# Performance work log

Hardware: AMD Instinct MI355X
Metric: run time of the kernel (lower is better)

Reference implementation:

```python
import jax, jax.numpy as jnp
import numpy as np

D_MODEL = 1024
T = 4096

def setup_inputs() -> dict:
    key = jax.random.key(0)
    k1, k2, k3 = jax.random.split(key, 3)
    x = jax.random.normal(k1, (T, D_MODEL), dtype=jnp.float32)
    # original uses torch.rand (uniform [0,1)) for params
    Wqk = jax.random.uniform(k2, (D_MODEL, D_MODEL), dtype=jnp.float32)
    Wov = jax.random.uniform(k3, (D_MODEL, D_MODEL), dtype=jnp.float32)
    return {"x": x, "Wqk": Wqk, "Wov": Wov}

def reference(x, Wqk, Wov):
    Tcur = x.shape[0]
    # scores = softmax(x @ Wqk @ x^T + causal_mask)
    q = x @ Wqk                              # [T, d]
    logits = q @ x.T                         # [T, T]
    causal = jnp.tril(jnp.ones((Tcur, Tcur), dtype=bool))
    logits = jnp.where(causal, logits, -jnp.inf)
    attn = jax.nn.softmax(logits, axis=-1)   # [T, T]
    out = (attn @ x) @ Wov                   # [T, d]
    return out
```

## Files before the change

kernel.cpp:

```cpp
#include <hip/hip_runtime.h>
#include <hip/hip_fp16.h>

#define T_DIM 4096
#define D_DIM 1024

typedef _Float16 f16;
typedef _Float16 f16x4 __attribute__((ext_vector_type(4)));
typedef _Float16 f16x8 __attribute__((ext_vector_type(8)));
typedef float f32x4 __attribute__((ext_vector_type(4)));

#define GAS __attribute__((address_space(1)))
#define LAS __attribute__((address_space(3)))

__global__ void split4(const float* __restrict__ in, f16* __restrict__ hi,
                       f16* __restrict__ lo) {
    int i = (blockIdx.x * 256 + threadIdx.x) * 4;
    float4 v = *(const float4*)(in + i);
    float vv[4] = {v.x, v.y, v.z, v.w};
    f16x4 h, l;
#pragma unroll
    for (int j = 0; j < 4; ++j) {
        f16 hh = (f16)vv[j];
        h[j] = hh;
        l[j] = (f16)(vv[j] - (float)hh);
    }
    *(f16x4*)(hi + i) = h;
    *(f16x4*)(lo + i) = l;
}

__global__ void transpose_split(const float* __restrict__ in, f16* __restrict__ hi,
                                f16* __restrict__ lo, int R, int C) {
    __shared__ float t[32][33];
    int tx = threadIdx.x & 31;
    int ty = threadIdx.x >> 5;
#pragma unroll
    for (int q = 0; q < 4; ++q) {
        int r = blockIdx.y * 32 + ty + q * 8;
        int c = blockIdx.x * 32 + tx;
        t[ty + q * 8][tx] = in[(size_t)r * C + c];
    }
    __syncthreads();
#pragma unroll
    for (int q = 0; q < 4; ++q) {
        int c = blockIdx.x * 32 + ty + q * 8;
        int r = blockIdx.y * 32 + tx;
        float v = t[tx][ty + q * 8];
        size_t idx = (size_t)c * R + r;
        f16 h = (f16)v;
        hi[idx] = h;
        lo[idx] = (f16)(v - (float)h);
    }
}

template <int ROWS>
__device__ __forceinline__ void stage_tile(const f16* __restrict__ src, int ld,
                                           f16* lds_tile, int w, int l) {
    constexpr int ITER = (ROWS * 4) / 256;
#pragma unroll
    for (int q = 0; q < ITER; ++q) {
        int p = q * 256 + w * 64 + l;
        int r = p >> 2;
        int c = (p & 3) ^ ((r >> 1) & 3);
        const f16* g = src + r * ld + c * 8;
        f16* d = lds_tile + (q * 256 + w * 64) * 8;
        __builtin_amdgcn_global_load_lds((const GAS void*)g, (LAS void*)d, 16, 0, 0);
    }
}

template <int N>
__device__ __forceinline__ void vm_wait() {
    static_assert(N == 0 || N == 3 || N == 6 || N == 8, "unsupported vmcnt");
    if constexpr (N == 0) asm volatile("s_waitcnt vmcnt(0)" ::: "memory");
    else if constexpr (N == 3) asm volatile("s_waitcnt vmcnt(3)" ::: "memory");
    else if constexpr (N == 6) asm volatile("s_waitcnt vmcnt(6)" ::: "memory");
    else if constexpr (N == 8) asm volatile("s_waitcnt vmcnt(8)" ::: "memory");
}

template <int TM, int TN, bool SPLIT3, int OUT_MODE, bool CAUSAL_SKIP,
          bool KCAP_CAUSAL, bool REVY>
__global__ __launch_bounds__(256) void gemm_nt(
    const f16* __restrict__ Ah, const f16* __restrict__ Al,
    const f16* __restrict__ Bh, const f16* __restrict__ Bl,
    float* __restrict__ Cf, f16* __restrict__ Ch, f16* __restrict__ Cl,
    int M, int N, int K) {
    const int by = REVY ? (gridDim.y - 1 - blockIdx.y) : blockIdx.y;
    const int row0 = by * TM;
    const int col0 = blockIdx.x * TN;
    if (CAUSAL_SKIP) {
        if (col0 > row0 + TM - 1) return;
    }
    int Keff = K;
    if (KCAP_CAUSAL) {
        Keff = row0 + TM;
        if (Keff > K) Keff = K;
    }

    constexpr int TILE_A = TM * 32;
    constexpr int TILE_B = TN * 32;
    constexpr int BUFSZ = (SPLIT3 ? 2 : 1) * (TILE_A + TILE_B);
    constexpr int M_REP = TM / 32;
    constexpr int N_REP = TN / 32;
    constexpr int LPS = (SPLIT3 ? 2 : 1) * (TM + TN) / 64;
    __shared__ f16 lds[2 * BUFSZ];

    const int tid = threadIdx.x;
    const int w = tid >> 6, l = tid & 63;
    const int wm = w >> 1, wn = w & 1;
    const int lr = l & 15;
    const int kg = l >> 4;
    const int cswz = kg ^ ((lr >> 1) & 3);
    const int aoff = (wm * (TM / 2) + lr) * 32 + cswz * 8;
    const int boff = (wn * (TN / 2) + lr) * 32 + cswz * 8;

    const f16* Asrc = Ah + (size_t)row0 * K;
    const f16* Bsrc = Bh + (size_t)col0 * K;
    const f16* Asrc_l = SPLIT3 ? Al + (size_t)row0 * K : nullptr;
    const f16* Bsrc_l = SPLIT3 ? Bl + (size_t)col0 * K : nullptr;

    auto stage_all = [&](int buf, int k0) {
        f16* base = lds + buf * BUFSZ;
        stage_tile<TM>(Asrc + k0, K, base, w, l);
        stage_tile<TN>(Bsrc + k0, K, base + TILE_A, w, l);
        if constexpr (SPLIT3) {
            stage_tile<TM>(Asrc_l + k0, K, base + TILE_A + TILE_B, w, l);
            stage_tile<TN>(Bsrc_l + k0, K, base + 2 * TILE_A + TILE_B, w, l);
        }
    };

    f32x4 acc[M_REP][N_REP] = {};

    const int nsteps = Keff >> 5;

    stage_all(0, 0);
    stage_all(1, 32);

    int cur = 0;
    for (int i = 0; i < nsteps; ++i) {
        if (i + 1 < nsteps) vm_wait<LPS>(); else vm_wait<0>();
        __builtin_amdgcn_sched_barrier(0);
        __builtin_amdgcn_s_barrier();
        __builtin_amdgcn_sched_barrier(0);

        const f16* base = lds + cur * BUFSZ;
        const f16* Ah_t = base;
        const f16* Bh_t = base + TILE_A;
        const f16* Al_t = base + TILE_A + TILE_B;
        const f16* Bl_t = base + 2 * TILE_A + TILE_B;

        f16x8 ah[M_REP], bh[N_REP], al[M_REP], bl[N_REP];
#pragma unroll
        for (int m = 0; m < M_REP; ++m) {
            ah[m] = *(const f16x8*)&Ah_t[aoff + m * 512];
            if constexpr (SPLIT3) al[m] = *(const f16x8*)&Al_t[aoff + m * 512];
        }
#pragma unroll
        for (int n = 0; n < N_REP; ++n) {
            bh[n] = *(const f16x8*)&Bh_t[boff + n * 512];
            if constexpr (SPLIT3) bl[n] = *(const f16x8*)&Bl_t[boff + n * 512];
        }

        asm volatile("s_waitcnt lgkmcnt(0)" ::: "memory");
        __builtin_amdgcn_sched_barrier(0);
        __builtin_amdgcn_s_barrier();
        __builtin_amdgcn_sched_barrier(0);

        if (i + 2 < nsteps) stage_all(cur, (i + 2) * 32);

#pragma unroll
        for (int m = 0; m < M_REP; ++m)
#pragma unroll
            for (int n = 0; n < N_REP; ++n) {
                acc[m][n] = __builtin_amdgcn_mfma_f32_16x16x32_f16(ah[m], bh[n],
                                                                   acc[m][n], 0, 0, 0);
                if constexpr (SPLIT3) {
                    acc[m][n] = __builtin_amdgcn_mfma_f32_16x16x32_f16(
                        al[m], bh[n], acc[m][n], 0, 0, 0);
                    acc[m][n] = __builtin_amdgcn_mfma_f32_16x16x32_f16(
                        ah[m], bl[n], acc[m][n], 0, 0, 0);
                }
            }

        cur ^= 1;
    }

#pragma unroll
    for (int m = 0; m < M_REP; ++m)
#pragma unroll
        for (int n = 0; n < N_REP; ++n)
#pragma unroll
            for (int j = 0; j < 4; ++j) {
                int row = row0 + wm * (TM / 2) + m * 16 + kg * 4 + j;
                int col = col0 + wn * (TN / 2) + n * 16 + lr;
                size_t idx = (size_t)row * N + col;
                float v = acc[m][n][j];
                if constexpr (OUT_MODE == 0) {
                    Cf[idx] = v;
                } else if constexpr (OUT_MODE == 1) {
                    f16 h = (f16)v;
                    Ch[idx] = h;
                    Cl[idx] = (f16)(v - (float)h);
                } else {
                    Ch[idx] = (f16)v;
                }
            }
}

__global__ void softmax_causal(const float* __restrict__ L, f16* __restrict__ A) {
    const int i = blockIdx.x;
    const int n = i + 1;
    const int tid = threadIdx.x;
    const float* row = L + (size_t)i * T_DIM;
    f16* arow = A + (size_t)i * T_DIM;

    float m = -INFINITY, s = 0.f;
    for (int j = tid; j < n; j += 256) {
        float v = row[j];
        if (v > m) {
            s = s * __expf(m - v) + 1.f;
            m = v;
        } else {
            s += __expf(v - m);
        }
    }

    __shared__ float sm[256], ss[256];
    sm[tid] = m;
    ss[tid] = s;
    __syncthreads();
    for (int o = 128; o > 0; o >>= 1) {
        if (tid < o) {
            float m1 = sm[tid], s1 = ss[tid];
            float m2 = sm[tid + o], s2 = ss[tid + o];
            float M = fmaxf(m1, m2);
            float S = (M == -INFINITY) ? 0.f
                                       : s1 * __expf(m1 - M) + s2 * __expf(m2 - M);
            sm[tid] = M;
            ss[tid] = S;
        }
        __syncthreads();
    }
    const float M = sm[0];
    const float inv = 1.f / ss[0];

    const int jmax = ((i >> 7) + 1) << 7;
    for (int j = tid; j < jmax; j += 256) {
        float v = (j < n) ? __expf(row[j] - M) * inv : 0.f;
        arow[j] = (f16)v;
    }
}

extern "C" void kernel_launch(void* const* d_in, const int* in_sizes, int n_in,
                              void* d_out, int out_size, void* d_ws, size_t ws_size,
                              hipStream_t stream) {
    (void)in_sizes; (void)n_in; (void)out_size; (void)ws_size;
    const float* x = (const float*)d_in[0];
    const float* wqk = (const float*)d_in[1];
    const float* wov = (const float*)d_in[2];
    float* out = (float*)d_out;
    char* ws = (char*)d_ws;
    const size_t MB = 1024 * 1024;

    f16* x_hi    = (f16*)(ws + 0 * MB);
    f16* x_lo    = (f16*)(ws + 8 * MB);
    f16* wqkT_hi = (f16*)(ws + 16 * MB);
    f16* wqkT_lo = (f16*)(ws + 18 * MB);
    f16* wovT_hi = (f16*)(ws + 20 * MB);
    f16* wovT_lo = (f16*)(ws + 22 * MB);
    f16* xT_hi   = (f16*)(ws + 24 * MB);
    f16* xT_lo   = (f16*)(ws + 32 * MB);
    f16* q_hi    = (f16*)(ws + 40 * MB);
    f16* q_lo    = (f16*)(ws + 48 * MB);
    f16* z_hi    = (f16*)(ws + 56 * MB);
    f16* attn    = (f16*)(ws + 64 * MB);
    float* logit = (float*)(ws + 96 * MB);

    split4<<<(T_DIM * D_DIM) / 1024, 256, 0, stream>>>(x, x_hi, x_lo);
    transpose_split<<<dim3(D_DIM / 32, D_DIM / 32), 256, 0, stream>>>(
        wqk, wqkT_hi, wqkT_lo, D_DIM, D_DIM);
    transpose_split<<<dim3(D_DIM / 32, D_DIM / 32), 256, 0, stream>>>(
        wov, wovT_hi, wovT_lo, D_DIM, D_DIM);
    transpose_split<<<dim3(D_DIM / 32, T_DIM / 32), 256, 0, stream>>>(
        x, xT_hi, xT_lo, T_DIM, D_DIM);

    gemm_nt<128, 64, true, 1, false, false, false>
        <<<dim3(D_DIM / 64, T_DIM / 128), 256, 0, stream>>>(
            x_hi, x_lo, wqkT_hi, wqkT_lo, nullptr, q_hi, q_lo, T_DIM, D_DIM, D_DIM);

    gemm_nt<128, 128, true, 0, true, false, false>
        <<<dim3(T_DIM / 128, T_DIM / 128), 256, 0, stream>>>(
            q_hi, q_lo, x_hi, x_lo, logit, nullptr, nullptr, T_DIM, T_DIM, D_DIM);

    softmax_causal<<<T_DIM, 256, 0, stream>>>(logit, attn);

    gemm_nt<128, 64, false, 2, false, true, true>
        <<<dim3(D_DIM / 64, T_DIM / 128), 256, 0, stream>>>(
            attn, nullptr, xT_hi, nullptr, nullptr, z_hi, nullptr, T_DIM, D_DIM, T_DIM);

    gemm_nt<128, 64, false, 0, false, false, false>
        <<<dim3(D_DIM / 64, T_DIM / 128), 256, 0, stream>>>(
            z_hi, nullptr, wovT_hi, nullptr, out, nullptr, nullptr, T_DIM, D_DIM, D_DIM);
}
```

Baseline: 283.8 us.

## Add triple-buffered LDS pipeline and BK=64 tiles to GEMM kernels

Parameterizes the GEMM on K-tile depth and buffer count. With three buffers, the prefetch two steps ahead writes a buffer nobody is reading, so the second barrier per step is dropped. The two non-split GEMMs move to BK=64 with a wider XOR swizzle, halving the barrier count per K. The unused low half of the x transpose is no longer written. In exchange, LDS use per block rises, which may lower occupancy, especially for the split3 Q GEMM with three buffers.

After: 270.4 us. 1.05x faster.

```diff
diff --git a/kernel.cpp b/kernel.cpp
--- a/kernel.cpp
+++ b/kernel.cpp
@@ -48,19 +48,21 @@
         size_t idx = (size_t)c * R + r;
         f16 h = (f16)v;
         hi[idx] = h;
-        lo[idx] = (f16)(v - (float)h);
-    }
-}
-
-template <int ROWS>
+        if (lo) lo[idx] = (f16)(v - (float)h);
+    }
+}
+
+template <int ROWS, int BK>
 __device__ __forceinline__ void stage_tile(const f16* __restrict__ src, int ld,
                                            f16* lds_tile, int w, int l) {
-    constexpr int ITER = (ROWS * 4) / 256;
+    constexpr int CH = BK / 8;
+    constexpr int ITER = (ROWS * BK) / 2048;
 #pragma unroll
     for (int q = 0; q < ITER; ++q) {
         int p = q * 256 + w * 64 + l;
-        int r = p >> 2;
-        int c = (p & 3) ^ ((r >> 1) & 3);
+        int r = p / CH;
+        int c0 = p % CH;
+        int c = (BK == 32) ? (c0 ^ ((r >> 1) & 3)) : (c0 ^ (r & 7));
         const f16* g = src + r * ld + c * 8;
         f16* d = lds_tile + (q * 256 + w * 64) * 8;
         __builtin_amdgcn_global_load_lds((const GAS void*)g, (LAS void*)d, 16, 0, 0);
@@ -76,13 +78,14 @@
     else if constexpr (N == 8) asm volatile("s_waitcnt vmcnt(8)" ::: "memory");
 }
 
-template <int TM, int TN, bool SPLIT3, int OUT_MODE, bool CAUSAL_SKIP,
-          bool KCAP_CAUSAL, bool REVY>
+template <int TM, int TN, int BK, int NBUF, bool SPLIT3, int OUT_MODE,
+          bool CAUSAL_SKIP, bool KCAP_CAUSAL, bool REVY>
 __global__ __launch_bounds__(256) void gemm_nt(
     const f16* __restrict__ Ah, const f16* __restrict__ Al,
     const f16* __restrict__ Bh, const f16* __restrict__ Bl,
     float* __restrict__ Cf, f16* __restrict__ Ch, f16* __restrict__ Cl,
     int M, int N, int K) {
+    static_assert(NBUF == 3 || BK == 32, "NBUF=2 schedule assumes BK=32");
     const int by = REVY ? (gridDim.y - 1 - blockIdx.y) : blockIdx.y;
     const int row0 = by * TM;
     const int col0 = blockIdx.x * TN;
@@ -95,22 +98,21 @@
         if (Keff > K) Keff = K;
     }
 
-    constexpr int TILE_A = TM * 32;
-    constexpr int TILE_B = TN * 32;
+    constexpr int TILE_A = TM * BK;
+    constexpr int TILE_B = TN * BK;
     constexpr int BUFSZ = (SPLIT3 ? 2 : 1) * (TILE_A + TILE_B);
     constexpr int M_REP = TM / 32;
     constexpr int N_REP = TN / 32;
-    constexpr int LPS = (SPLIT3 ? 2 : 1) * (TM + TN) / 64;
-    __shared__ f16 lds[2 * BUFSZ];
+    constexpr int LPS = (SPLIT3 ? 2 : 1) * (TM + TN) * BK / 2048;
+    __shared__ f16 lds[NBUF * BUFSZ];
 
     const int tid = threadIdx.x;
     const int w = tid >> 6, l = tid & 63;
     const int wm = w >> 1, wn = w & 1;
     const int lr = l & 15;
     const int kg = l >> 4;
-    const int cswz = kg ^ ((lr >> 1) & 3);
-    const int aoff = (wm * (TM / 2) + lr) * 32 + cswz * 8;
-    const int boff = (wn * (TN / 2) + lr) * 32 + cswz * 8;
+    const int arow = (wm * (TM / 2) + lr) * BK;
+    const int brow = (wn * (TN / 2) + lr) * BK;
 
     const f16* Asrc = Ah + (size_t)row0 * K;
     const f16* Bsrc = Bh + (size_t)col0 * K;
@@ -119,20 +121,20 @@
 
     auto stage_all = [&](int buf, int k0) {
         f16* base = lds + buf * BUFSZ;
-        stage_tile<TM>(Asrc + k0, K, base, w, l);
-        stage_tile<TN>(Bsrc + k0, K, base + TILE_A, w, l);
+        stage_tile<TM, BK>(Asrc + k0, K, base, w, l);
+        stage_tile<TN, BK>(Bsrc + k0, K, base + TILE_A, w, l);
         if constexpr (SPLIT3) {
-            stage_tile<TM>(Asrc_l + k0, K, base + TILE_A + TILE_B, w, l);
-            stage_tile<TN>(Bsrc_l + k0, K, base + 2 * TILE_A + TILE_B, w, l);
+            stage_tile<TM, BK>(Asrc_l + k0, K, base + TILE_A + TILE_B, w, l);
+            stage_tile<TN, BK>(Bsrc_l + k0, K, base + 2 * TILE_A + TILE_B, w, l);
         }
     };
 
     f32x4 acc[M_REP][N_REP] = {};
 
-    const int nsteps = Keff >> 5;
+    const int nsteps = Keff / BK;
 
     stage_all(0, 0);
-    stage_all(1, 32);
+    stage_all(1, BK);
 
     int cur = 0;
     for (int i = 0; i < nsteps; ++i) {
@@ -147,40 +149,53 @@
         const f16* Al_t = base + TILE_A + TILE_B;
         const f16* Bl_t = base + 2 * TILE_A + TILE_B;
 
-        f16x8 ah[M_REP], bh[N_REP], al[M_REP], bl[N_REP];
-#pragma unroll
-        for (int m = 0; m < M_REP; ++m) {
-            ah[m] = *(const f16x8*)&Ah_t[aoff + m * 512];
-            if constexpr (SPLIT3) al[m] = *(const f16x8*)&Al_t[aoff + m * 512];
+#pragma unroll
+        for (int kk = 0; kk < BK / 32; ++kk) {
+            const int chA = (BK == 32) ? (kg ^ ((lr >> 1) & 3))
+                                       : ((kk * 4 + kg) ^ (lr & 7));
+            const int aoff = arow + chA * 8;
+            const int boff = brow + chA * 8;
+
+            f16x8 ah[M_REP], bh[N_REP], al[M_REP], bl[N_REP];
+#pragma unroll
+            for (int m = 0; m < M_REP; ++m) {
+                ah[m] = *(const f16x8*)&Ah_t[aoff + m * 16 * BK];
+                if constexpr (SPLIT3) al[m] = *(const f16x8*)&Al_t[aoff + m * 16 * BK];
+            }
+#pragma unroll
+            for (int n = 0; n < N_REP; ++n) {
+                bh[n] = *(const f16x8*)&Bh_t[boff + n * 16 * BK];
+                if constexpr (SPLIT3) bl[n] = *(const f16x8*)&Bl_t[boff + n * 16 * BK];
+            }
+
+            if constexpr (NBUF == 2) {
+                asm volatile("s_waitcnt lgkmcnt(0)" ::: "memory");
+                __builtin_amdgcn_sched_barrier(0);
+                __builtin_amdgcn_s_barrier();
+                __builtin_amdgcn_sched_barrier(0);
+            }
+
+            if (kk == 0 && i + 2 < nsteps) {
+                const int stg = (NBUF == 2) ? cur : ((cur == 0) ? 2 : cur - 1);
+                stage_all(stg, (i + 2) * BK);
+            }
+
+#pragma unroll
+            for (int m = 0; m < M_REP; ++m)
+#pragma unroll
+                for (int n = 0; n < N_REP; ++n) {
+                    acc[m][n] = __builtin_amdgcn_mfma_f32_16x16x32_f16(
+                        ah[m], bh[n], acc[m][n], 0, 0, 0);
+                    if constexpr (SPLIT3) {
+                        acc[m][n] = __builtin_amdgcn_mfma_f32_16x16x32_f16(
+                            al[m], bh[n], acc[m][n], 0, 0, 0);
+                        acc[m][n] = __builtin_amdgcn_mfma_f32_16x16x32_f16(
+                            ah[m], bl[n], acc[m][n], 0, 0, 0);
+                    }
+                }
         }
-#pragma unroll
-        for (int n = 0; n < N_REP; ++n) {
-            bh[n] = *(const f16x8*)&Bh_t[boff + n * 512];
-            if constexpr (SPLIT3) bl[n] = *(const f16x8*)&Bl_t[boff + n * 512];
-        }
-
-        asm volatile("s_waitcnt lgkmcnt(0)" ::: "memory");
-        __builtin_amdgcn_sched_barrier(0);
-        __builtin_amdgcn_s_barrier();
-        __builtin_amdgcn_sched_barrier(0);
-
-        if (i + 2 < nsteps) stage_all(cur, (i + 2) * 32);
-
-#pragma unroll
-        for (int m = 0; m < M_REP; ++m)
-#pragma unroll
-            for (int n = 0; n < N_REP; ++n) {
-                acc[m][n] = __builtin_amdgcn_mfma_f32_16x16x32_f16(ah[m], bh[n],
-                                                                   acc[m][n], 0, 0, 0);
-                if constexpr (SPLIT3) {
-                    acc[m][n] = __builtin_amdgcn_mfma_f32_16x16x32_f16(
-                        al[m], bh[n], acc[m][n], 0, 0, 0);
-                    acc[m][n] = __builtin_amdgcn_mfma_f32_16x16x32_f16(
-                        ah[m], bl[n], acc[m][n], 0, 0, 0);
-                }
-            }
-
-        cur ^= 1;
+
+        cur = (cur + 1 == NBUF) ? 0 : cur + 1;
     }
 
 #pragma unroll
@@ -267,7 +282,6 @@
     f16* wovT_hi = (f16*)(ws + 20 * MB);
     f16* wovT_lo = (f16*)(ws + 22 * MB);
     f16* xT_hi   = (f16*)(ws + 24 * MB);
-    f16* xT_lo   = (f16*)(ws + 32 * MB);
     f16* q_hi    = (f16*)(ws + 40 * MB);
     f16* q_lo    = (f16*)(ws + 48 * MB);
     f16* z_hi    = (f16*)(ws + 56 * MB);
@@ -280,23 +294,23 @@
     transpose_split<<<dim3(D_DIM / 32, D_DIM / 32), 256, 0, stream>>>(
         wov, wovT_hi, wovT_lo, D_DIM, D_DIM);
     transpose_split<<<dim3(D_DIM / 32, T_DIM / 32), 256, 0, stream>>>(
-        x, xT_hi, xT_lo, T_DIM, D_DIM);
-
-    gemm_nt<128, 64, true, 1, false, false, false>
+        x, xT_hi, nullptr, T_DIM, D_DIM);
+
+    gemm_nt<128, 64, 32, 3, true, 1, false, false, false>
         <<<dim3(D_DIM / 64, T_DIM / 128), 256, 0, stream>>>(
             x_hi, x_lo, wqkT_hi, wqkT_lo, nullptr, q_hi, q_lo, T_DIM, D_DIM, D_DIM);
 
-    gemm_nt<128, 128, true, 0, true, false, false>
+    gemm_nt<128, 128, 32, 2, true, 0, true, false, false>
         <<<dim3(T_DIM / 128, T_DIM / 128), 256, 0, stream>>>(
             q_hi, q_lo, x_hi, x_lo, logit, nullptr, nullptr, T_DIM, T_DIM, D_DIM);
 
     softmax_causal<<<T_DIM, 256, 0, stream>>>(logit, attn);
 
-    gemm_nt<128, 64, false, 2, false, true, true>
+    gemm_nt<128, 64, 64, 3, false, 2, false, true, true>
         <<<dim3(D_DIM / 64, T_DIM / 128), 256, 0, stream>>>(
             attn, nullptr, xT_hi, nullptr, nullptr, z_hi, nullptr, T_DIM, D_DIM, T_DIM);
 
-    gemm_nt<128, 64, false, 0, false, false, false>
+    gemm_nt<128, 64, 64, 3, false, 0, false, false, false>
         <<<dim3(D_DIM / 64, T_DIM / 128), 256, 0, stream>>>(
             z_hi, nullptr, wovT_hi, nullptr, out, nullptr, nullptr, T_DIM, D_DIM, D_DIM);
 }
```
